# Performance work log

Hardware: AMD Instinct MI355X
Metric: run time of the kernel (lower is better)

Reference implementation:

```python
import jax, jax.numpy as jnp
import numpy as np

B, T, C = 8, 512, 1024
H, E = 16, 64          # n_head, head_dim; H*E == C
L = 2048               # cached (prefix) length in the KV cache


def setup_inputs() -> dict:
    key = jax.random.key(0)
    ks = jax.random.split(key, 6)
    scale = 0.02
    return {
        "x": jax.random.normal(ks[0], (B, T, C), jnp.float32),
        "k_cache": jax.random.normal(ks[1], (B, H, L, E), jnp.float32),
        "v_cache": jax.random.normal(ks[2], (B, H, L, E), jnp.float32),
        "Wqkv": jax.random.normal(ks[3], (C, 3 * C), jnp.float32) * scale,
        "bqkv": jnp.zeros((3 * C,), jnp.float32),
        "Wproj": jax.random.normal(ks[4], (C, C), jnp.float32) * scale,
        "bproj": jnp.zeros((C,), jnp.float32),
    }


def reference(x, k_cache, v_cache, Wqkv, bqkv, Wproj, bproj):
    qkv = x @ Wqkv + bqkv
    q, k, v = jnp.split(qkv, 3, axis=-1)

    def to_heads(t):
        return t.reshape(B, T, H, E).transpose(0, 2, 1, 3)

    q, k, v = to_heads(q), to_heads(k), to_heads(v)

    # append new k,v to the cache (kv_cache.update + get)
    k_full = jnp.concatenate([k_cache, k], axis=2)  # (B,H,L+T,E)
    v_full = jnp.concatenate([v_cache, v], axis=2)

    # manual self-attention with cache-offset causal mask: row i (global pos L+i)
    # may attend to cols j <= L+i  (bias[L:L+T, :L+T])
    att = jnp.einsum("bhte,bhse->bhts", q, k_full) * (1.0 / np.sqrt(E))
    i = jnp.arange(T)[:, None] + L
    j = jnp.arange(L + T)[None, :]
    att = jnp.where(j <= i, att, -jnp.inf)
    att = jax.nn.softmax(att, axis=-1)

    y = jnp.einsum("bhts,bhse->bhte", att, v_full)
    y = y.transpose(0, 2, 1, 3).reshape(B, T, C)
    return y @ Wproj + bproj
```

## Files before the change

### kernel.cpp

```cpp
#include <hip/hip_runtime.h>
#include <hip/hip_bf16.h>

typedef unsigned short u16;
typedef unsigned int u32;

constexpr int B_ = 8, T_ = 512, C_ = 1024, H_ = 16, E_ = 64, L_ = 2048;
constexpr int S_ = L_ + T_;

typedef __bf16 bf16x8 __attribute__((ext_vector_type(8)));
typedef float f32x4 __attribute__((ext_vector_type(4)));
typedef float f32x16 __attribute__((ext_vector_type(16)));

#define QSCALE 0.18033688011112042f

__device__ inline u16 f2bf(float f) {
  u32 u = __float_as_uint(f);
  u32 r = (u + 0x7fffu + ((u >> 16) & 1u)) >> 16;
  return (u16)r;
}

__device__ inline u32 pk2(float a, float b) {
  union { __hip_bfloat162 h; u32 u; } cv;
  cv.h = __float22bfloat162_rn(float2{a, b});
  return cv.u;
}

__device__ inline void pl32swap(u32& a, u32& b) {
  asm("v_permlane32_swap_b32 %0, %1" : "+v"(a), "+v"(b));
}

__device__ inline void gload_lds16(const u16* g, u16* l) {
  __builtin_amdgcn_global_load_lds(
      (const __attribute__((address_space(1))) u32*)g,
      (__attribute__((address_space(3))) u32*)l, 16, 0, 0);
}

__global__ __launch_bounds__(256) void convert_f32_bf16(const float* __restrict__ in,
                                                        u16* __restrict__ out) {
  const int i = blockIdx.x * 256 + threadIdx.x;
  const float4 a0 = ((const float4*)in)[i * 2];
  const float4 a1 = ((const float4*)in)[i * 2 + 1];
  uint4 p;
  p.x = pk2(a0.x, a0.y);
  p.y = pk2(a0.z, a0.w);
  p.z = pk2(a1.x, a1.y);
  p.w = pk2(a1.z, a1.w);
  ((uint4*)out)[i] = p;
}

__global__ __launch_bounds__(256) void transpose_f32_bf16(const float* __restrict__ in,
                                                          u16* __restrict__ out,
                                                          int R, int Ccols) {
  __shared__ u16 tile[64][65];
  const int r0 = blockIdx.y * 64;
  const int c0 = blockIdx.x * 64;
  const int tr = threadIdx.x >> 6;
  const int tc = threadIdx.x & 63;
#pragma unroll
  for (int i = 0; i < 16; ++i)
    tile[tr + i * 4][tc] = f2bf(in[(size_t)(r0 + tr + i * 4) * Ccols + c0 + tc]);
  __syncthreads();
#pragma unroll
  for (int i = 0; i < 16; ++i)
    out[(size_t)(c0 + tr + i * 4) * R + r0 + tc] = tile[tc][tr + i * 4];
}

__global__ __launch_bounds__(256) void prep_kv(const float* __restrict__ kc,
                                               const float* __restrict__ vc,
                                               u16* __restrict__ Km,
                                               u16* __restrict__ Vtm) {
  __shared__ u16 vt[64 * 72];
  const int s0 = (blockIdx.x & 31) * 64;
  const int bh = blockIdx.x >> 5;
  const int tid = threadIdx.x;
  const int srow = tid >> 2;
  const int eq = (tid & 3) * 16;

  {
    const float* kp = kc + ((size_t)bh * L_ + s0 + srow) * E_ + eq;
    float kv[16];
    *(float4*)(kv + 0) = *(const float4*)(kp + 0);
    *(float4*)(kv + 4) = *(const float4*)(kp + 4);
    *(float4*)(kv + 8) = *(const float4*)(kp + 8);
    *(float4*)(kv + 12) = *(const float4*)(kp + 12);
    uint4 p0, p1;
    p0.x = pk2(kv[0], kv[1]);
    p0.y = pk2(kv[2], kv[3]);
    p0.z = pk2(kv[4], kv[5]);
    p0.w = pk2(kv[6], kv[7]);
    p1.x = pk2(kv[8], kv[9]);
    p1.y = pk2(kv[10], kv[11]);
    p1.z = pk2(kv[12], kv[13]);
    p1.w = pk2(kv[14], kv[15]);
    u16* kd = Km + ((size_t)bh * S_ + s0 + srow) * E_ + eq;
    *(uint4*)kd = p0;
    *(uint4*)(kd + 8) = p1;
  }
  {
    const float* vp = vc + ((size_t)bh * L_ + s0 + srow) * E_ + eq;
    float vv[16];
    *(float4*)(vv + 0) = *(const float4*)(vp + 0);
    *(float4*)(vv + 4) = *(const float4*)(vp + 4);
    *(float4*)(vv + 8) = *(const float4*)(vp + 8);
    *(float4*)(vv + 12) = *(const float4*)(vp + 12);
    uint4 p0, p1;
    p0.x = pk2(vv[0], vv[1]);
    p0.y = pk2(vv[2], vv[3]);
    p0.z = pk2(vv[4], vv[5]);
    p0.w = pk2(vv[6], vv[7]);
    p1.x = pk2(vv[8], vv[9]);
    p1.y = pk2(vv[10], vv[11]);
    p1.z = pk2(vv[12], vv[13]);
    p1.w = pk2(vv[14], vv[15]);
    *(uint4*)(vt + srow * 72 + eq) = p0;
    *(uint4*)(vt + srow * 72 + eq + 8) = p1;
  }
  __syncthreads();
  {
    const int erow = tid >> 2;
    const int sq = (tid & 3) * 16;
    u16 o[16];
#pragma unroll
    for (int j = 0; j < 16; ++j) o[j] = vt[(sq + j) * 72 + erow];
    u16* vd = Vtm + ((size_t)bh * E_ + erow) * S_ + s0 + sq;
    *(uint4*)vd = *(uint4*)(o + 0);
    *(uint4*)(vd + 8) = *(uint4*)(o + 8);
  }
}

__global__ __launch_bounds__(256) void vtrans(const u16* __restrict__ vh,
                                              u16* __restrict__ Vtm) {
  __shared__ u16 vt[64 * 72];
  const int t0 = (blockIdx.x & 7) * 64;
  const int bh = blockIdx.x >> 3;
  const int tid = threadIdx.x;
  const int srow = tid >> 2;
  const int eq = (tid & 3) * 16;
  const u16* vp = vh + ((size_t)bh * T_ + t0 + srow) * E_ + eq;
  *(uint4*)(vt + srow * 72 + eq) = *(const uint4*)vp;
  *(uint4*)(vt + srow * 72 + eq + 8) = *(const uint4*)(vp + 8);
  __syncthreads();
  const int erow = tid >> 2;
  const int sq = (tid & 3) * 16;
  u16 o[16];
#pragma unroll
  for (int j = 0; j < 16; ++j) o[j] = vt[(sq + j) * 72 + erow];
  u16* vd = Vtm + ((size_t)bh * E_ + erow) * S_ + L_ + t0 + sq;
  *(uint4*)vd = *(uint4*)(o + 0);
  *(uint4*)(vd + 8) = *(uint4*)(o + 8);
}

template <int MODE>
__global__ __launch_bounds__(256) void gemm128(const u16* __restrict__ A,
                                               const u16* __restrict__ BT,
                                               const float* __restrict__ bias,
                                               u16* __restrict__ qh,
                                               u16* __restrict__ Km,
                                               u16* __restrict__ vout,
                                               float* __restrict__ outf,
                                               int M, int N, int K) {
  __shared__ __align__(16) u16 As[128 * 32];
  __shared__ __align__(16) u16 Bs[128 * 32];
  const int tid = threadIdx.x;
  const int lane = tid & 63;
  const int w = tid >> 6;
  const int m0 = blockIdx.y * 128;
  const int n0 = blockIdx.x * 128;
  const int wm = (w >> 1) * 64;
  const int wn = (w & 1) * 64;
  const int fm = lane & 15;
  const int fk = (lane >> 4) * 8;

  const int srow = w * 16 + (lane >> 2);
  const int scol = (lane & 3) * 8;
  const u16* Ag = A + (size_t)(m0 + srow) * K + scol;
  const u16* Bg = BT + (size_t)(n0 + srow) * K + scol;
  u16* AsU = As + w * 512;
  u16* BsU = Bs + w * 512;

  f32x4 acc[4][4];
#pragma unroll
  for (int i = 0; i < 4; ++i)
#pragma unroll
    for (int j = 0; j < 4; ++j) acc[i][j] = f32x4{0.f, 0.f, 0.f, 0.f};

  for (int k0 = 0; k0 < K; k0 += 32) {
    gload_lds16(Ag, AsU);
    gload_lds16(Ag + (size_t)64 * K, AsU + 2048);
    gload_lds16(Bg, BsU);
    gload_lds16(Bg + (size_t)64 * K, BsU + 2048);
    Ag += 32;
    Bg += 32;
    __syncthreads();
    bf16x8 af[4], bf[4];
#pragma unroll
    for (int i = 0; i < 4; ++i)
      af[i] = *(const bf16x8*)(As + (wm + i * 16 + fm) * 32 + fk);
#pragma unroll
    for (int j = 0; j < 4; ++j)
      bf[j] = *(const bf16x8*)(Bs + (wn + j * 16 + fm) * 32 + fk);
#pragma unroll
    for (int i = 0; i < 4; ++i)
#pragma unroll
      for (int j = 0; j < 4; ++j)
        acc[i][j] = __builtin_amdgcn_mfma_f32_16x16x32_bf16(af[i], bf[j], acc[i][j], 0, 0, 0);
    __syncthreads();
  }

  const int rbase = (lane >> 4) * 4;
  const int cbase = lane & 15;
#pragma unroll
  for (int i = 0; i < 4; ++i)
#pragma unroll
    for (int j = 0; j < 4; ++j) {
      const int n = n0 + wn + j * 16 + cbase;
      const float bv = bias[n];
#pragma unroll
      for (int r = 0; r < 4; ++r) {
        const int m = m0 + wm + i * 16 + rbase + r;
        const float v = acc[i][j][r] + bv;
        if (MODE == 0) {
          const int seg = n >> 10;
          const int c = n & 1023;
          const int e = c & 63;
          const int bhh = ((m >> 9) * H_) + (c >> 6);
          const int t = m & 511;
          if (seg == 0)
            qh[((size_t)bhh * T_ + t) * E_ + e] = f2bf(v * QSCALE);
          else if (seg == 1)
            Km[((size_t)bhh * S_ + L_ + t) * E_ + e] = f2bf(v);
          else
            vout[((size_t)bhh * T_ + t) * E_ + e] = f2bf(v);
        } else {
          outf[(size_t)m * N + n] = v;
        }
      }
    }
}

__global__ __launch_bounds__(512, 4) void attn_v6(const u16* __restrict__ qh,
                                                  const u16* __restrict__ Km,
                                                  const u16* __restrict__ Vtm,
                                                  u16* __restrict__ y2) {
  __shared__ __align__(16) u16 smem[32768];
  u16* KsB = smem;
  u16* VtsB = smem + 16384;

  const int tid = threadIdx.x;
  const int lane = tid & 63;
  const int w = tid >> 6;
  const int wq = w & 3;
  const int par = w >> 2;
  const int bh = blockIdx.x & 127;
  const int qt = blockIdx.x >> 7;
  const int h = bh & (H_ - 1);
  const int b = bh >> 4;
  const int t0 = qt * 128;

  const int ln = lane & 31;
  const int hi = lane >> 5;
  const int swz = ln & 7;

  const u16* qbase = qh + ((size_t)bh * T_ + t0 + wq * 32 + ln) * E_;
  bf16x8 qf[4];
#pragma unroll
  for (int et = 0; et < 4; ++et)
    qf[et] = *(const bf16x8*)(qbase + et * 16 + hi * 8);

  const int tq = tid & 255;
  const int sp = tid >> 8;
  const int srow = tq >> 2;
  const int su = (tq & 3) * 2;
  const u16* kg = Km + ((size_t)bh * S_ + srow) * E_ + su * 8;
  const u16* vg = Vtm + ((size_t)bh * E_ + srow) * S_ + su * 8;
  const int st0 = srow * 64 + ((su ^ (srow & 7)) * 8);
  const int st1 = srow * 64 + (((su + 1) ^ (srow & 7)) * 8);

  f32x16 Yt[2], lacc, zero16;
#pragma unroll
  for (int i = 0; i < 16; ++i) {
    Yt[0][i] = 0.f;
    Yt[1][i] = 0.f;
    lacc[i] = 0.f;
    zero16[i] = 0.f;
  }

  const bf16x8 ones = {(__bf16)1.f, (__bf16)1.f, (__bf16)1.f, (__bf16)1.f,
                       (__bf16)1.f, (__bf16)1.f, (__bf16)1.f, (__bf16)1.f};

  const int qmin_w = L_ + t0 + wq * 32;
  const int qpos = qmin_w + ln;
  const int nchunk = (L_ + t0 + 128) >> 6;
  const int npair = nchunk >> 1;

  {
    const size_t ko = (size_t)sp * 64 * E_;
    const int vo = sp * 64;
    uint4 kr0 = *(const uint4*)(kg + ko);
    uint4 kr1 = *(const uint4*)(kg + ko + 8);
    uint4 vr0 = *(const uint4*)(vg + vo);
    uint4 vr1 = *(const uint4*)(vg + vo + 8);
    u16* kd = KsB + sp * 4096;
    u16* vd = VtsB + sp * 4096;
    *(uint4*)(kd + st0) = kr0;
    *(uint4*)(kd + st1) = kr1;
    *(uint4*)(vd + st0) = vr0;
    *(uint4*)(vd + st1) = vr1;
  }
  __syncthreads();

  for (int i = 0; i < npair; ++i) {
    const int hlf = i & 1;
    const int cs = 2 * (i + 1) + sp;
    const bool more = cs < nchunk;
    uint4 kr0, kr1, vr0, vr1;
    if (more) {
      const size_t ko = (size_t)cs * 64 * E_;
      const int vo = cs * 64;
      kr0 = *(const uint4*)(kg + ko);
      kr1 = *(const uint4*)(kg + ko + 8);
      vr0 = *(const uint4*)(vg + vo);
      vr1 = *(const uint4*)(vg + vo + 8);
    }

    const int cmy = 2 * i + par;
    const int sbase = cmy << 6;
    if (sbase <= qmin_w + 31) {
      const u16* ks = KsB + (hlf * 2 + par) * 4096;
      const u16* vs = VtsB + (hlf * 2 + par) * 4096;
      bf16x8 pa[4];
#pragma unroll
      for (int kb = 0; kb < 2; ++kb) {
        f32x16 s;
#pragma unroll
        for (int et = 0; et < 4; ++et) {
          const bf16x8 kf = *(const bf16x8*)(
              ks + (kb * 32 + ln) * 64 + (((et * 2 + hi) ^ swz) * 8));
          s = __builtin_amdgcn_mfma_f32_32x32x16_bf16(kf, qf[et],
                                                      et == 0 ? zero16 : s, 0, 0, 0);
        }

        if (sbase + 63 > qmin_w) {
          const int mb = sbase + kb * 32 + hi * 4;
#pragma unroll
          for (int r = 0; r < 16; ++r) {
            const int keypos = mb + (r & 3) + 8 * (r >> 2);
            if (keypos > qpos) s[r] = -1e30f;
          }
        }

#pragma unroll
        for (int r = 0; r < 16; ++r) s[r] = exp2f(s[r]);

#pragma unroll
        for (int t = 0; t < 2; ++t) {
          u32 x0 = pk2(s[8 * t + 0], s[8 * t + 1]);
          u32 y0 = pk2(s[8 * t + 4], s[8 * t + 5]);
          u32 x1 = pk2(s[8 * t + 2], s[8 * t + 3]);
          u32 y1 = pk2(s[8 * t + 6], s[8 * t + 7]);
          pl32swap(x0, y0);
          pl32swap(x1, y1);
          union { u32 u[4]; bf16x8 v; } pu;
          pu.u[0] = x0;
          pu.u[1] = x1;
          pu.u[2] = y0;
          pu.u[3] = y1;
          pa[kb * 2 + t] = pu.v;
        }
      }

#pragma unroll
      for (int t = 0; t < 4; ++t)
        lacc = __builtin_amdgcn_mfma_f32_32x32x16_bf16(ones, pa[t], lacc, 0, 0, 0);

#pragma unroll
      for (int eb = 0; eb < 2; ++eb)
#pragma unroll
        for (int t = 0; t < 4; ++t) {
          const bf16x8 vf = *(const bf16x8*)(
              vs + (eb * 32 + ln) * 64 + (((t * 2 + hi) ^ swz) * 8));
          Yt[eb] = __builtin_amdgcn_mfma_f32_32x32x16_bf16(vf, pa[t], Yt[eb], 0, 0, 0);
        }
    }

    if (more) {
      u16* kd = KsB + ((hlf ^ 1) * 2 + sp) * 4096;
      u16* vd = VtsB + ((hlf ^ 1) * 2 + sp) * 4096;
      *(uint4*)(kd + st0) = kr0;
      *(uint4*)(kd + st1) = kr1;
      *(uint4*)(vd + st0) = vr0;
      *(uint4*)(vd + st1) = vr1;
    }
    __syncthreads();
  }

  float* red = (float*)smem;
  if (par == 1) {
    float* rp = red + ((size_t)(wq * 64 + lane)) * 34;
#pragma unroll
    for (int i = 0; i < 16; ++i) rp[i] = Yt[0][i];
#pragma unroll
    for (int i = 0; i < 16; ++i) rp[16 + i] = Yt[1][i];
    rp[32] = lacc[0];
  }
  __syncthreads();
  if (par == 0) {
    const float* rp = red + ((size_t)(wq * 64 + lane)) * 34;
#pragma unroll
    for (int i = 0; i < 16; ++i) Yt[0][i] += rp[i];
#pragma unroll
    for (int i = 0; i < 16; ++i) Yt[1][i] += rp[16 + i];
    const float rl = 1.f / (lacc[0] + rp[32]);

    const int t_out = t0 + wq * 32 + ln;
    u16* yp = y2 + ((size_t)b * T_ + t_out) * C_ + h * E_ + hi * 4;
#pragma unroll
    for (int eb = 0; eb < 2; ++eb)
#pragma unroll
      for (int g = 0; g < 4; ++g) {
        uint2 st;
        st.x = pk2(Yt[eb][4 * g + 0] * rl, Yt[eb][4 * g + 1] * rl);
        st.y = pk2(Yt[eb][4 * g + 2] * rl, Yt[eb][4 * g + 3] * rl);
        *(uint2*)(yp + eb * 32 + g * 8) = st;
      }
  }
}

extern "C" void kernel_launch(void* const* d_in, const int* in_sizes, int n_in,
                              void* d_out, int out_size, void* d_ws, size_t ws_size,
                              hipStream_t stream) {
  const float* x = (const float*)d_in[0];
  const float* kc = (const float*)d_in[1];
  const float* vc = (const float*)d_in[2];
  const float* Wqkv = (const float*)d_in[3];
  const float* bqkv = (const float*)d_in[4];
  const float* Wproj = (const float*)d_in[5];
  const float* bproj = (const float*)d_in[6];
  float* out = (float*)d_out;

  u16* qh = (u16*)d_ws;
  u16* y2 = qh + 4194304;
  u16* xb = y2 + 4194304;
  u16* WqT = xb + 4194304;
  u16* WpT = WqT + 3145728;
  u16* Km = WpT + 1048576;
  u16* Vtm = Km + 20971520;

  convert_f32_bf16<<<dim3(2048), 256, 0, stream>>>(x, xb);
  transpose_f32_bf16<<<dim3(48, 16), 256, 0, stream>>>(Wqkv, WqT, 1024, 3072);
  transpose_f32_bf16<<<dim3(16, 16), 256, 0, stream>>>(Wproj, WpT, 1024, 1024);
  prep_kv<<<dim3(128 * 32), 256, 0, stream>>>(kc, vc, Km, Vtm);

  gemm128<0><<<dim3(24, 32), 256, 0, stream>>>(xb, WqT, bqkv, qh, Km, y2, nullptr,
                                               4096, 3072, 1024);
  vtrans<<<dim3(128 * 8), 256, 0, stream>>>(y2, Vtm);

  attn_v6<<<dim3(512), 512, 0, stream>>>(qh, Km, Vtm, y2);

  gemm128<1><<<dim3(8, 32), 256, 0, stream>>>(y2, WpT, bproj, nullptr, nullptr,
                                              nullptr, out, 4096, 1024, 1024);
}
```

Baseline: 355.4 us.

## Merge prep kernels, use inline bf16 pack asm, restructure attention without key split

Three preprocessing kernels (x conversion, two weight transposes, KV cache prep) are merged into one launch that dispatches on block index, saving launch overhead. The bf16 packing helper now uses the v_cvt_pk_bf16_f32 instruction directly. The attention kernel drops its two-way key-chunk split across 8 waves, so 4 waves each process both 64-key chunks per round. This removes the final LDS reduction and a barrier but halves the threads per block, which lowers intra-block parallelism and latency hiding.

```diff
diff --git a/kernel.cpp b/kernel.cpp
--- a/kernel.cpp
+++ b/kernel.cpp
@@ -20,9 +20,9 @@
 }
 
 __device__ inline u32 pk2(float a, float b) {
-  union { __hip_bfloat162 h; u32 u; } cv;
-  cv.h = __float22bfloat162_rn(float2{a, b});
-  return cv.u;
+  u32 r;
+  asm("v_cvt_pk_bf16_f32 %0, %1, %2" : "=v"(r) : "v"(a), "v"(b));
+  return r;
 }
 
 __device__ inline void pl32swap(u32& a, u32& b) {
@@ -35,44 +35,61 @@
       (__attribute__((address_space(3))) u32*)l, 16, 0, 0);
 }
 
-__global__ __launch_bounds__(256) void convert_f32_bf16(const float* __restrict__ in,
-                                                        u16* __restrict__ out) {
-  const int i = blockIdx.x * 256 + threadIdx.x;
-  const float4 a0 = ((const float4*)in)[i * 2];
-  const float4 a1 = ((const float4*)in)[i * 2 + 1];
-  uint4 p;
-  p.x = pk2(a0.x, a0.y);
-  p.y = pk2(a0.z, a0.w);
-  p.z = pk2(a1.x, a1.y);
-  p.w = pk2(a1.z, a1.w);
-  ((uint4*)out)[i] = p;
-}
-
-__global__ __launch_bounds__(256) void transpose_f32_bf16(const float* __restrict__ in,
-                                                          u16* __restrict__ out,
-                                                          int R, int Ccols) {
-  __shared__ u16 tile[64][65];
-  const int r0 = blockIdx.y * 64;
-  const int c0 = blockIdx.x * 64;
-  const int tr = threadIdx.x >> 6;
-  const int tc = threadIdx.x & 63;
-#pragma unroll
-  for (int i = 0; i < 16; ++i)
-    tile[tr + i * 4][tc] = f2bf(in[(size_t)(r0 + tr + i * 4) * Ccols + c0 + tc]);
-  __syncthreads();
-#pragma unroll
-  for (int i = 0; i < 16; ++i)
-    out[(size_t)(c0 + tr + i * 4) * R + r0 + tc] = tile[tc][tr + i * 4];
-}
-
-__global__ __launch_bounds__(256) void prep_kv(const float* __restrict__ kc,
-                                               const float* __restrict__ vc,
-                                               u16* __restrict__ Km,
-                                               u16* __restrict__ Vtm) {
-  __shared__ u16 vt[64 * 72];
-  const int s0 = (blockIdx.x & 31) * 64;
-  const int bh = blockIdx.x >> 5;
+__global__ __launch_bounds__(256) void prep_all(const float* __restrict__ x,
+                                                u16* __restrict__ xb,
+                                                const float* __restrict__ Wqkv,
+                                                u16* __restrict__ WqT,
+                                                const float* __restrict__ Wproj,
+                                                u16* __restrict__ WpT,
+                                                const float* __restrict__ kc,
+                                                const float* __restrict__ vc,
+                                                u16* __restrict__ Km,
+                                                u16* __restrict__ Vtm) {
+  __shared__ __align__(16) u16 sh[64 * 72];
+  const int bid = blockIdx.x;
   const int tid = threadIdx.x;
+
+  if (bid < 2048) {
+    const int i = bid * 256 + tid;
+    const float4 a0 = ((const float4*)x)[i * 2];
+    const float4 a1 = ((const float4*)x)[i * 2 + 1];
+    uint4 p;
+    p.x = pk2(a0.x, a0.y);
+    p.y = pk2(a0.z, a0.w);
+    p.z = pk2(a1.x, a1.y);
+    p.w = pk2(a1.z, a1.w);
+    ((uint4*)xb)[i] = p;
+    return;
+  }
+
+  if (bid < 3072) {
+    const float* in;
+    u16* out;
+    int R = 1024, Ccols, bx, by;
+    if (bid < 2816) {
+      in = Wqkv; out = WqT; Ccols = 3072;
+      bx = (bid - 2048) % 48; by = (bid - 2048) / 48;
+    } else {
+      in = Wproj; out = WpT; Ccols = 1024;
+      bx = (bid - 2816) % 16; by = (bid - 2816) / 16;
+    }
+    const int r0 = by * 64;
+    const int c0 = bx * 64;
+    const int tr = tid >> 6;
+    const int tc = tid & 63;
+#pragma unroll
+    for (int i = 0; i < 16; ++i)
+      sh[(tr + i * 4) * 65 + tc] = f2bf(in[(size_t)(r0 + tr + i * 4) * Ccols + c0 + tc]);
+    __syncthreads();
+#pragma unroll
+    for (int i = 0; i < 16; ++i)
+      out[(size_t)(c0 + tr + i * 4) * R + r0 + tc] = sh[tc * 65 + tr + i * 4];
+    return;
+  }
+
+  const int pb = bid - 3072;
+  const int s0 = (pb & 31) * 64;
+  const int bh = pb >> 5;
   const int srow = tid >> 2;
   const int eq = (tid & 3) * 16;
 
@@ -112,8 +129,8 @@
     p1.y = pk2(vv[10], vv[11]);
     p1.z = pk2(vv[12], vv[13]);
     p1.w = pk2(vv[14], vv[15]);
-    *(uint4*)(vt + srow * 72 + eq) = p0;
-    *(uint4*)(vt + srow * 72 + eq + 8) = p1;
+    *(uint4*)(sh + srow * 72 + eq) = p0;
+    *(uint4*)(sh + srow * 72 + eq + 8) = p1;
   }
   __syncthreads();
   {
@@ -121,7 +138,7 @@
     const int sq = (tid & 3) * 16;
     u16 o[16];
 #pragma unroll
-    for (int j = 0; j < 16; ++j) o[j] = vt[(sq + j) * 72 + erow];
+    for (int j = 0; j < 16; ++j) o[j] = sh[(sq + j) * 72 + erow];
     u16* vd = Vtm + ((size_t)bh * E_ + erow) * S_ + s0 + sq;
     *(uint4*)vd = *(uint4*)(o + 0);
     *(uint4*)(vd + 8) = *(uint4*)(o + 8);
@@ -238,19 +255,16 @@
     }
 }
 
-__global__ __launch_bounds__(512, 4) void attn_v6(const u16* __restrict__ qh,
+__global__ __launch_bounds__(256, 2) void attn_v7(const u16* __restrict__ qh,
                                                   const u16* __restrict__ Km,
                                                   const u16* __restrict__ Vtm,
                                                   u16* __restrict__ y2) {
-  __shared__ __align__(16) u16 smem[32768];
-  u16* KsB = smem;
-  u16* VtsB = smem + 16384;
+  __shared__ __align__(16) u16 KsB[2][2][4096];
+  __shared__ __align__(16) u16 VtsB[2][2][4096];
 
   const int tid = threadIdx.x;
   const int lane = tid & 63;
   const int w = tid >> 6;
-  const int wq = w & 3;
-  const int par = w >> 2;
   const int bh = blockIdx.x & 127;
   const int qt = blockIdx.x >> 7;
   const int h = bh & (H_ - 1);
@@ -261,16 +275,14 @@
   const int hi = lane >> 5;
   const int swz = ln & 7;
 
-  const u16* qbase = qh + ((size_t)bh * T_ + t0 + wq * 32 + ln) * E_;
+  const u16* qbase = qh + ((size_t)bh * T_ + t0 + w * 32 + ln) * E_;
   bf16x8 qf[4];
 #pragma unroll
   for (int et = 0; et < 4; ++et)
     qf[et] = *(const bf16x8*)(qbase + et * 16 + hi * 8);
 
-  const int tq = tid & 255;
-  const int sp = tid >> 8;
-  const int srow = tq >> 2;
-  const int su = (tq & 3) * 2;
+  const int srow = tid >> 2;
+  const int su = (tid & 3) * 2;
   const u16* kg = Km + ((size_t)bh * S_ + srow) * E_ + su * 8;
   const u16* vg = Vtm + ((size_t)bh * E_ + srow) * S_ + su * 8;
   const int st0 = srow * 64 + ((su ^ (srow & 7)) * 8);
@@ -288,142 +300,127 @@
   const bf16x8 ones = {(__bf16)1.f, (__bf16)1.f, (__bf16)1.f, (__bf16)1.f,
                        (__bf16)1.f, (__bf16)1.f, (__bf16)1.f, (__bf16)1.f};
 
-  const int qmin_w = L_ + t0 + wq * 32;
+  const int qmin_w = L_ + t0 + w * 32;
   const int qpos = qmin_w + ln;
-  const int nchunk = (L_ + t0 + 128) >> 6;
-  const int npair = nchunk >> 1;
-
-  {
-    const size_t ko = (size_t)sp * 64 * E_;
-    const int vo = sp * 64;
-    uint4 kr0 = *(const uint4*)(kg + ko);
-    uint4 kr1 = *(const uint4*)(kg + ko + 8);
-    uint4 vr0 = *(const uint4*)(vg + vo);
-    uint4 vr1 = *(const uint4*)(vg + vo + 8);
-    u16* kd = KsB + sp * 4096;
-    u16* vd = VtsB + sp * 4096;
-    *(uint4*)(kd + st0) = kr0;
-    *(uint4*)(kd + st1) = kr1;
-    *(uint4*)(vd + st0) = vr0;
-    *(uint4*)(vd + st1) = vr1;
+  const int nround = (L_ + t0 + 128) >> 7;
+
+#pragma unroll
+  for (int sub = 0; sub < 2; ++sub) {
+    const size_t ko = (size_t)sub * 64 * E_;
+    const int vo = sub * 64;
+    const uint4 k0 = *(const uint4*)(kg + ko);
+    const uint4 k1 = *(const uint4*)(kg + ko + 8);
+    const uint4 v0 = *(const uint4*)(vg + vo);
+    const uint4 v1 = *(const uint4*)(vg + vo + 8);
+    *(uint4*)(&KsB[0][sub][st0]) = k0;
+    *(uint4*)(&KsB[0][sub][st1]) = k1;
+    *(uint4*)(&VtsB[0][sub][st0]) = v0;
+    *(uint4*)(&VtsB[0][sub][st1]) = v1;
   }
   __syncthreads();
 
-  for (int i = 0; i < npair; ++i) {
-    const int hlf = i & 1;
-    const int cs = 2 * (i + 1) + sp;
-    const bool more = cs < nchunk;
-    uint4 kr0, kr1, vr0, vr1;
+  for (int r = 0; r < nround; ++r) {
+    const int hlf = r & 1;
+    const bool more = (r + 1 < nround);
+    uint4 nk[2][2], nv[2][2];
     if (more) {
-      const size_t ko = (size_t)cs * 64 * E_;
-      const int vo = cs * 64;
-      kr0 = *(const uint4*)(kg + ko);
-      kr1 = *(const uint4*)(kg + ko + 8);
-      vr0 = *(const uint4*)(vg + vo);
-      vr1 = *(const uint4*)(vg + vo + 8);
-    }
-
-    const int cmy = 2 * i + par;
-    const int sbase = cmy << 6;
-    if (sbase <= qmin_w + 31) {
-      const u16* ks = KsB + (hlf * 2 + par) * 4096;
-      const u16* vs = VtsB + (hlf * 2 + par) * 4096;
-      bf16x8 pa[4];
-#pragma unroll
-      for (int kb = 0; kb < 2; ++kb) {
-        f32x16 s;
-#pragma unroll
-        for (int et = 0; et < 4; ++et) {
-          const bf16x8 kf = *(const bf16x8*)(
-              ks + (kb * 32 + ln) * 64 + (((et * 2 + hi) ^ swz) * 8));
-          s = __builtin_amdgcn_mfma_f32_32x32x16_bf16(kf, qf[et],
-                                                      et == 0 ? zero16 : s, 0, 0, 0);
-        }
-
-        if (sbase + 63 > qmin_w) {
-          const int mb = sbase + kb * 32 + hi * 4;
-#pragma unroll
-          for (int r = 0; r < 16; ++r) {
-            const int keypos = mb + (r & 3) + 8 * (r >> 2);
-            if (keypos > qpos) s[r] = -1e30f;
+#pragma unroll
+      for (int sub = 0; sub < 2; ++sub) {
+        const int c = 2 * (r + 1) + sub;
+        const size_t ko = (size_t)c * 64 * E_;
+        nk[sub][0] = *(const uint4*)(kg + ko);
+        nk[sub][1] = *(const uint4*)(kg + ko + 8);
+        nv[sub][0] = *(const uint4*)(vg + c * 64);
+        nv[sub][1] = *(const uint4*)(vg + c * 64 + 8);
+      }
+    }
+
+#pragma unroll
+    for (int sub = 0; sub < 2; ++sub) {
+      const int sbase = (2 * r + sub) << 6;
+      if (sbase <= qmin_w + 31) {
+        const u16* ks = KsB[hlf][sub];
+        const u16* vs = VtsB[hlf][sub];
+        bf16x8 pa[4];
+#pragma unroll
+        for (int kb = 0; kb < 2; ++kb) {
+          f32x16 s;
+#pragma unroll
+          for (int et = 0; et < 4; ++et) {
+            const bf16x8 kf = *(const bf16x8*)(
+                ks + (kb * 32 + ln) * 64 + (((et * 2 + hi) ^ swz) * 8));
+            s = __builtin_amdgcn_mfma_f32_32x32x16_bf16(kf, qf[et],
+                                                        et == 0 ? zero16 : s, 0, 0, 0);
+          }
+
+          if (sbase + 63 > qmin_w) {
+            const int mb = sbase + kb * 32 + hi * 4;
+#pragma unroll
+            for (int rr = 0; rr < 16; ++rr) {
+              const int keypos = mb + (rr & 3) + 8 * (rr >> 2);
+              if (keypos > qpos) s[rr] = -1e30f;
+            }
+          }
+
+#pragma unroll
+          for (int rr = 0; rr < 16; ++rr) s[rr] = exp2f(s[rr]);
+
+#pragma unroll
+          for (int t = 0; t < 2; ++t) {
+            u32 x0 = pk2(s[8 * t + 0], s[8 * t + 1]);
+            u32 y0 = pk2(s[8 * t + 4], s[8 * t + 5]);
+            u32 x1 = pk2(s[8 * t + 2], s[8 * t + 3]);
+            u32 y1 = pk2(s[8 * t + 6], s[8 * t + 7]);
+            pl32swap(x0, y0);
+            pl32swap(x1, y1);
+            union { u32 u[4]; bf16x8 v; } pu;
+            pu.u[0] = x0;
+            pu.u[1] = x1;
+            pu.u[2] = y0;
+            pu.u[3] = y1;
+            pa[kb * 2 + t] = pu.v;
           }
         }
 
 #pragma unroll
-        for (int r = 0; r < 16; ++r) s[r] = exp2f(s[r]);
-
-#pragma unroll
-        for (int t = 0; t < 2; ++t) {
-          u32 x0 = pk2(s[8 * t + 0], s[8 * t + 1]);
-          u32 y0 = pk2(s[8 * t + 4], s[8 * t + 5]);
-          u32 x1 = pk2(s[8 * t + 2], s[8 * t + 3]);
-          u32 y1 = pk2(s[8 * t + 6], s[8 * t + 7]);
-          pl32swap(x0, y0);
-          pl32swap(x1, y1);
-          union { u32 u[4]; bf16x8 v; } pu;
-          pu.u[0] = x0;
-          pu.u[1] = x1;
-          pu.u[2] = y0;
-          pu.u[3] = y1;
-          pa[kb * 2 + t] = pu.v;
-        }
+        for (int t = 0; t < 4; ++t)
+          lacc = __builtin_amdgcn_mfma_f32_32x32x16_bf16(ones, pa[t], lacc, 0, 0, 0);
+
+#pragma unroll
+        for (int eb = 0; eb < 2; ++eb)
+#pragma unroll
+          for (int t = 0; t < 4; ++t) {
+            const bf16x8 vf = *(const bf16x8*)(
+                vs + (eb * 32 + ln) * 64 + (((t * 2 + hi) ^ swz) * 8));
+            Yt[eb] = __builtin_amdgcn_mfma_f32_32x32x16_bf16(vf, pa[t], Yt[eb], 0, 0, 0);
+          }
       }
-
-#pragma unroll
-      for (int t = 0; t < 4; ++t)
-        lacc = __builtin_amdgcn_mfma_f32_32x32x16_bf16(ones, pa[t], lacc, 0, 0, 0);
-
-#pragma unroll
-      for (int eb = 0; eb < 2; ++eb)
-#pragma unroll
-        for (int t = 0; t < 4; ++t) {
-          const bf16x8 vf = *(const bf16x8*)(
-              vs + (eb * 32 + ln) * 64 + (((t * 2 + hi) ^ swz) * 8));
-          Yt[eb] = __builtin_amdgcn_mfma_f32_32x32x16_bf16(vf, pa[t], Yt[eb], 0, 0, 0);
-        }
     }
 
     if (more) {
-      u16* kd = KsB + ((hlf ^ 1) * 2 + sp) * 4096;
-      u16* vd = VtsB + ((hlf ^ 1) * 2 + sp) * 4096;
-      *(uint4*)(kd + st0) = kr0;
-      *(uint4*)(kd + st1) = kr1;
-      *(uint4*)(vd + st0) = vr0;
-      *(uint4*)(vd + st1) = vr1;
+#pragma unroll
+      for (int sub = 0; sub < 2; ++sub) {
+        *(uint4*)(&KsB[hlf ^ 1][sub][st0]) = nk[sub][0];
+        *(uint4*)(&KsB[hlf ^ 1][sub][st1]) = nk[sub][1];
+        *(uint4*)(&VtsB[hlf ^ 1][sub][st0]) = nv[sub][0];
+        *(uint4*)(&VtsB[hlf ^ 1][sub][st1]) = nv[sub][1];
+      }
     }
     __syncthreads();
   }
 
-  float* red = (float*)smem;
-  if (par == 1) {
-    float* rp = red + ((size_t)(wq * 64 + lane)) * 34;
-#pragma unroll
-    for (int i = 0; i < 16; ++i) rp[i] = Yt[0][i];
-#pragma unroll
-    for (int i = 0; i < 16; ++i) rp[16 + i] = Yt[1][i];
-    rp[32] = lacc[0];
-  }
-  __syncthreads();
-  if (par == 0) {
-    const float* rp = red + ((size_t)(wq * 64 + lane)) * 34;
-#pragma unroll
-    for (int i = 0; i < 16; ++i) Yt[0][i] += rp[i];
-#pragma unroll
-    for (int i = 0; i < 16; ++i) Yt[1][i] += rp[16 + i];
-    const float rl = 1.f / (lacc[0] + rp[32]);
-
-    const int t_out = t0 + wq * 32 + ln;
-    u16* yp = y2 + ((size_t)b * T_ + t_out) * C_ + h * E_ + hi * 4;
-#pragma unroll
-    for (int eb = 0; eb < 2; ++eb)
-#pragma unroll
-      for (int g = 0; g < 4; ++g) {
-        uint2 st;
-        st.x = pk2(Yt[eb][4 * g + 0] * rl, Yt[eb][4 * g + 1] * rl);
-        st.y = pk2(Yt[eb][4 * g + 2] * rl, Yt[eb][4 * g + 3] * rl);
-        *(uint2*)(yp + eb * 32 + g * 8) = st;
-      }
-  }
+  const float rl = 1.f / lacc[0];
+  const int t_out = t0 + w * 32 + ln;
+  u16* yp = y2 + ((size_t)b * T_ + t_out) * C_ + h * E_ + hi * 4;
+#pragma unroll
+  for (int eb = 0; eb < 2; ++eb)
+#pragma unroll
+    for (int g = 0; g < 4; ++g) {
+      uint2 st;
+      st.x = pk2(Yt[eb][4 * g + 0] * rl, Yt[eb][4 * g + 1] * rl);
+      st.y = pk2(Yt[eb][4 * g + 2] * rl, Yt[eb][4 * g + 3] * rl);
+      *(uint2*)(yp + eb * 32 + g * 8) = st;
+    }
 }
 
 extern "C" void kernel_launch(void* const* d_in, const int* in_sizes, int n_in,
@@ -446,16 +443,14 @@
   u16* Km = WpT + 1048576;
   u16* Vtm = Km + 20971520;
 
-  convert_f32_bf16<<<dim3(2048), 256, 0, stream>>>(x, xb);
-  transpose_f32_bf16<<<dim3(48, 16), 256, 0, stream>>>(Wqkv, WqT, 1024, 3072);
-  transpose_f32_bf16<<<dim3(16, 16), 256, 0, stream>>>(Wproj, WpT, 1024, 1024);
-  prep_kv<<<dim3(128 * 32), 256, 0, stream>>>(kc, vc, Km, Vtm);
+  prep_all<<<dim3(7168), 256, 0, stream>>>(x, xb, Wqkv, WqT, Wproj, WpT,
+                                           kc, vc, Km, Vtm);
 
   gemm128<0><<<dim3(24, 32), 256, 0, stream>>>(xb, WqT, bqkv, qh, Km, y2, nullptr,
                                                4096, 3072, 1024);
   vtrans<<<dim3(128 * 8), 256, 0, stream>>>(y2, Vtm);
 
-  attn_v6<<<dim3(512), 512, 0, stream>>>(qh, Km, Vtm, y2);
+  attn_v7<<<dim3(512), 256, 0, stream>>>(qh, Km, Vtm, y2);
 
   gemm128<1><<<dim3(8, 32), 256, 0, stream>>>(y2, WpT, bproj, nullptr, nullptr,
                                               nullptr, out, 4096, 1024, 1024);
```

Measured after the change: 371.1 us. +4.4%, slower.
